# Optimization experiments

Measured on AMD Instinct MI355X. Metric: run time of the kernel, lower is better.

## Reference

```python
import jax, jax.numpy as jnp
import numpy as np

D_MODEL = 1024
N_HEADS = 8
D_KEYS = 128
D_LLM = 4096


def setup_inputs() -> dict:
    key = jax.random.key(0)
    ks = jax.random.split(key, 12)
    B, L, S = 8, 1024, 1000
    dk = D_KEYS * N_HEADS  # 1024
    inp = {
        "target_embedding": jax.random.normal(ks[0], (B, L, D_MODEL), jnp.float32),
        "source_embedding": jax.random.normal(ks[1], (S, D_LLM), jnp.float32),
        "value_embedding": jax.random.normal(ks[2], (S, D_LLM), jnp.float32),
        # nn.Linear weights are [out_features, in_features]
        "Wq": jax.random.normal(ks[3], (dk, D_MODEL), jnp.float32) * 0.02,
        "bq": jnp.zeros((dk,), jnp.float32),
        "Wk": jax.random.normal(ks[4], (dk, D_LLM), jnp.float32) * 0.02,
        "bk": jnp.zeros((dk,), jnp.float32),
        "Wv": jax.random.normal(ks[5], (dk, D_LLM), jnp.float32) * 0.02,
        "bv": jnp.zeros((dk,), jnp.float32),
        "Wo": jax.random.normal(ks[6], (D_LLM, dk), jnp.float32) * 0.02,
        "bo": jnp.zeros((D_LLM,), jnp.float32),
    }
    return inp


def reference(target_embedding, source_embedding, value_embedding,
              Wq, bq, Wk, bk, Wv, bv, Wo, bo):
    B, L, _ = target_embedding.shape
    S, _ = source_embedding.shape
    H, E = N_HEADS, D_KEYS
    # projections (torch Linear: x @ W.T + b)
    q = (target_embedding @ Wq.T + bq).reshape(B, L, H, E)
    k = (source_embedding @ Wk.T + bk).reshape(S, H, E)
    v = (value_embedding @ Wv.T + bv).reshape(S, H, E)
    scale = 1.0 / np.sqrt(E).astype(np.float32)
    # cross-attention of B*L queries over S shared prototypes
    scores = jnp.einsum('blhe,she->bhls', q, k)  # [B,H,L,S]
    A = jax.nn.softmax(scale * scores, axis=-1)  # dropout is identity in eval
    out = jnp.einsum('bhls,she->blhe', A, v).reshape(B, L, H * E)
    return out @ Wo.T + bo  # [B, L, D_LLM]
```

## Files before the change

### kernel.cpp

```cpp
#include <hip/hip_runtime.h>
#include <hip/hip_bf16.h>


typedef __attribute__((ext_vector_type(8))) short short8;
typedef __attribute__((ext_vector_type(4))) short short4v;
typedef __attribute__((ext_vector_type(4))) float f32x4;
typedef __attribute__((ext_vector_type(4))) int int4v;

#define DEVINL static __device__ __forceinline__

DEVINL unsigned short f2bf(float f) {
  union { float f; unsigned u; } v; v.f = f;
  unsigned r = v.u + 0x7FFFu + ((v.u >> 16) & 1u);
  return (unsigned short)(r >> 16);
}

DEVINL f32x4 zero4() { f32x4 z; z[0] = 0.f; z[1] = 0.f; z[2] = 0.f; z[3] = 0.f; return z; }
DEVINL short8 zero8() { short8 z; z[0]=0; z[1]=0; z[2]=0; z[3]=0; z[4]=0; z[5]=0; z[6]=0; z[7]=0; return z; }

DEVINL void load_lds16(const unsigned short* g, unsigned short* l) {
  __builtin_amdgcn_global_load_lds(
      (const __attribute__((address_space(1))) void*)g,
      (__attribute__((address_space(3))) void*)l, 16, 0, 0);
}

__global__ __launch_bounds__(256)
void cvt3_bf16(const float* __restrict__ s0, unsigned short* __restrict__ d0, int n0,
               const float* __restrict__ s1, unsigned short* __restrict__ d1, int n1,
               const float* __restrict__ s2, unsigned short* __restrict__ d2, int n2)
{
  int idx = (blockIdx.x * 256 + threadIdx.x) * 8;
  const float* s; unsigned short* d; int rel = idx;
  if (rel < n0) { s = s0; d = d0; }
  else {
    rel -= n0;
    if (rel < n1) { s = s1; d = d1; }
    else { rel -= n1; if (rel >= n2) return; s = s2; d = d2; }
  }
  f32x4 x0 = *(const f32x4*)(s + rel);
  f32x4 x1 = *(const f32x4*)(s + rel + 4);
  short8 o;
#pragma unroll
  for (int j = 0; j < 4; j++) { o[j] = (short)f2bf(x0[j]); o[4 + j] = (short)f2bf(x1[j]); }
  *(short8*)(d + rel) = o;
}

template<bool C_BF16>
__global__ __launch_bounds__(256)
void gemm_bb(const unsigned short* __restrict__ A,
             const unsigned short* __restrict__ B,
             const float* __restrict__ bias, float cscale, void* __restrict__ C_,
             int M, int N, int K)
{
  __shared__ unsigned short As[4096];
  __shared__ unsigned short Bs[4096];
  const int t = threadIdx.x;
  const int lane = t & 63, w = t >> 6;
  const int wm = w >> 1, wn = w & 1;
  const int l15 = lane & 15, l4 = lane >> 4;
  const int m0 = blockIdx.y * 128, n0 = blockIdx.x * 128;

  const int srow = w * 32 + (lane >> 2);
  const int scol = (lane & 3) * 8;
  const unsigned short* Ap = A + (size_t)(m0 + srow) * K + scol;
  const unsigned short* Bp = B + (size_t)(n0 + srow) * K + scol;
  unsigned short* AsW = &As[w * 1024];
  unsigned short* BsW = &Bs[w * 1024];

  f32x4 acc[4][4];
#pragma unroll
  for (int i = 0; i < 4; i++)
#pragma unroll
    for (int j = 0; j < 4; j++) acc[i][j] = zero4();

  for (int k0 = 0; k0 < K; k0 += 32) {
    if (k0) __syncthreads();
    load_lds16(Ap + k0, AsW);
    load_lds16(Ap + k0 + (size_t)16 * K, AsW + 512);
    load_lds16(Bp + k0, BsW);
    load_lds16(Bp + k0 + (size_t)16 * K, BsW + 512);
    __syncthreads();

    short8 af[4], bf[4];
#pragma unroll
    for (int mt = 0; mt < 4; mt++)
      af[mt] = *(const short8*)&As[(wm * 64 + mt * 16 + l15) * 32 + l4 * 8];
#pragma unroll
    for (int nt = 0; nt < 4; nt++)
      bf[nt] = *(const short8*)&Bs[(wn * 64 + nt * 16 + l15) * 32 + l4 * 8];
#pragma unroll
    for (int mt = 0; mt < 4; mt++)
#pragma unroll
      for (int nt = 0; nt < 4; nt++)
        acc[mt][nt] = __builtin_amdgcn_mfma_f32_16x16x32_bf16(af[mt], bf[nt], acc[mt][nt], 0, 0, 0);
  }

#pragma unroll
  for (int nt = 0; nt < 4; nt++) {
    const int col = n0 + wn * 64 + nt * 16 + l15;
    const float bvv = bias[col];
#pragma unroll
    for (int mt = 0; mt < 4; mt++) {
#pragma unroll
      for (int j = 0; j < 4; j++) {
        const int row = m0 + wm * 64 + mt * 16 + l4 * 4 + j;
        const float val = (acc[mt][nt][j] + bvv) * cscale;
        if constexpr (C_BF16)
          ((unsigned short*)C_)[(size_t)row * N + col] = f2bf(val);
        else
          ((float*)C_)[(size_t)row * N + col] = val;
      }
    }
  }
}

template<bool A_BF16, bool C_BF16, bool C_T>
__global__ __launch_bounds__(256)
void gemm_bt(const void* __restrict__ A_, const float* __restrict__ B,
             const float* __restrict__ bias, float cscale, void* __restrict__ C_,
             int M, int N, int K)
{
  __shared__ unsigned short As[128][40];
  __shared__ unsigned short Bs[128][40];
  const int t = threadIdx.x;
  const int lane = t & 63, w = t >> 6;
  const int wm = w >> 1, wn = w & 1;
  const int l15 = lane & 15, l4 = lane >> 4;
  const int m0 = blockIdx.y * 128, n0 = blockIdx.x * 128;
  const int srow = t >> 1, scol = (t & 1) * 16;

  f32x4 acc[4][4];
#pragma unroll
  for (int i = 0; i < 4; i++)
#pragma unroll
    for (int j = 0; j < 4; j++) acc[i][j] = zero4();

  const int am = m0 + srow;
  const int bn = n0 + srow;

  for (int k0 = 0; k0 < K; k0 += 32) {
    short8 av0, av1, bv0, bv1;
    if constexpr (A_BF16) {
      const unsigned short* A = (const unsigned short*)A_;
      if (am < M) {
        const unsigned short* p = A + (size_t)am * K + k0 + scol;
        av0 = *(const short8*)p;
        av1 = *(const short8*)(p + 8);
      } else { av0 = zero8(); av1 = zero8(); }
    } else {
      const float* A = (const float*)A_;
      if (am < M) {
        const float* p = A + (size_t)am * K + k0 + scol;
        f32x4 x0 = *(const f32x4*)(p);
        f32x4 x1 = *(const f32x4*)(p + 4);
        f32x4 x2 = *(const f32x4*)(p + 8);
        f32x4 x3 = *(const f32x4*)(p + 12);
#pragma unroll
        for (int i = 0; i < 4; i++) {
          av0[i]     = (short)f2bf(x0[i]);
          av0[4 + i] = (short)f2bf(x1[i]);
          av1[i]     = (short)f2bf(x2[i]);
          av1[4 + i] = (short)f2bf(x3[i]);
        }
      } else { av0 = zero8(); av1 = zero8(); }
    }
    {
      const float* p = B + (size_t)bn * K + k0 + scol;
      f32x4 x0 = *(const f32x4*)(p);
      f32x4 x1 = *(const f32x4*)(p + 4);
      f32x4 x2 = *(const f32x4*)(p + 8);
      f32x4 x3 = *(const f32x4*)(p + 12);
#pragma unroll
      for (int i = 0; i < 4; i++) {
        bv0[i]     = (short)f2bf(x0[i]);
        bv0[4 + i] = (short)f2bf(x1[i]);
        bv1[i]     = (short)f2bf(x2[i]);
        bv1[4 + i] = (short)f2bf(x3[i]);
      }
    }
    __syncthreads();
    *(short8*)&As[srow][scol]     = av0;
    *(short8*)&As[srow][scol + 8] = av1;
    *(short8*)&Bs[srow][scol]     = bv0;
    *(short8*)&Bs[srow][scol + 8] = bv1;
    __syncthreads();

    short8 af[4], bf[4];
#pragma unroll
    for (int mt = 0; mt < 4; mt++)
      af[mt] = *(const short8*)&As[wm * 64 + mt * 16 + l15][l4 * 8];
#pragma unroll
    for (int nt = 0; nt < 4; nt++)
      bf[nt] = *(const short8*)&Bs[wn * 64 + nt * 16 + l15][l4 * 8];
#pragma unroll
    for (int mt = 0; mt < 4; mt++)
#pragma unroll
      for (int nt = 0; nt < 4; nt++)
        acc[mt][nt] = __builtin_amdgcn_mfma_f32_16x16x32_bf16(af[mt], bf[nt], acc[mt][nt], 0, 0, 0);
  }

#pragma unroll
  for (int nt = 0; nt < 4; nt++) {
    const int col = n0 + wn * 64 + nt * 16 + l15;
    const float bvv = bias[col];
#pragma unroll
    for (int mt = 0; mt < 4; mt++) {
#pragma unroll
      for (int j = 0; j < 4; j++) {
        const int row = m0 + wm * 64 + mt * 16 + l4 * 4 + j;
        if (row < M) {
          float val = (acc[mt][nt][j] + bvv) * cscale;
          if constexpr (C_T)
            ((unsigned short*)C_)[(size_t)col * 1024 + row] = f2bf(val);
          else if constexpr (C_BF16)
            ((unsigned short*)C_)[(size_t)row * N + col] = f2bf(val);
          else
            ((float*)C_)[(size_t)row * N + col] = val;
        }
      }
    }
  }
}

__global__ __launch_bounds__(256)
void gemm_splitk_kv(const float* __restrict__ Src, const float* __restrict__ Val,
                    const float* __restrict__ Wk, const float* __restrict__ Wv,
                    float* __restrict__ Pt, int M, int N, int Ktot)
{
  __shared__ unsigned short As[128][40];
  __shared__ unsigned short Bs[128][40];
  const int t = threadIdx.x;
  const int lane = t & 63, w = t >> 6;
  const int wm = w >> 1, wn = w & 1;
  const int l15 = lane & 15, l4 = lane >> 4;
  const int m0 = blockIdx.y * 128, n0 = blockIdx.x * 128;
  const int srow = t >> 1, scol = (t & 1) * 16;

  const int split = blockIdx.z & 3;
  const int tensor = blockIdx.z >> 2;
  const float* A = tensor ? Val : Src;
  const float* B = tensor ? Wv : Wk;
  const int kchunk = Ktot >> 2;
  const int k_begin = split * kchunk;
  const int k_end = k_begin + kchunk;

  f32x4 acc[4][4];
#pragma unroll
  for (int i = 0; i < 4; i++)
#pragma unroll
    for (int j = 0; j < 4; j++) acc[i][j] = zero4();

  const int am = m0 + srow;
  const int bn = n0 + srow;

  for (int k0 = k_begin; k0 < k_end; k0 += 32) {
    short8 av0, av1, bv0, bv1;
    if (am < M) {
      const float* p = A + (size_t)am * Ktot + k0 + scol;
      f32x4 x0 = *(const f32x4*)(p);
      f32x4 x1 = *(const f32x4*)(p + 4);
      f32x4 x2 = *(const f32x4*)(p + 8);
      f32x4 x3 = *(const f32x4*)(p + 12);
#pragma unroll
      for (int i = 0; i < 4; i++) {
        av0[i]     = (short)f2bf(x0[i]);
        av0[4 + i] = (short)f2bf(x1[i]);
        av1[i]     = (short)f2bf(x2[i]);
        av1[4 + i] = (short)f2bf(x3[i]);
      }
    } else { av0 = zero8(); av1 = zero8(); }
    {
      const float* p = B + (size_t)bn * Ktot + k0 + scol;
      f32x4 x0 = *(const f32x4*)(p);
      f32x4 x1 = *(const f32x4*)(p + 4);
      f32x4 x2 = *(const f32x4*)(p + 8);
      f32x4 x3 = *(const f32x4*)(p + 12);
#pragma unroll
      for (int i = 0; i < 4; i++) {
        bv0[i]     = (short)f2bf(x0[i]);
        bv0[4 + i] = (short)f2bf(x1[i]);
        bv1[i]     = (short)f2bf(x2[i]);
        bv1[4 + i] = (short)f2bf(x3[i]);
      }
    }
    __syncthreads();
    *(short8*)&As[srow][scol]     = av0;
    *(short8*)&As[srow][scol + 8] = av1;
    *(short8*)&Bs[srow][scol]     = bv0;
    *(short8*)&Bs[srow][scol + 8] = bv1;
    __syncthreads();

    short8 af[4], bf[4];
#pragma unroll
    for (int mt = 0; mt < 4; mt++)
      af[mt] = *(const short8*)&As[wm * 64 + mt * 16 + l15][l4 * 8];
#pragma unroll
    for (int nt = 0; nt < 4; nt++)
      bf[nt] = *(const short8*)&Bs[wn * 64 + nt * 16 + l15][l4 * 8];
#pragma unroll
    for (int mt = 0; mt < 4; mt++)
#pragma unroll
      for (int nt = 0; nt < 4; nt++)
        acc[mt][nt] = __builtin_amdgcn_mfma_f32_16x16x32_bf16(af[mt], bf[nt], acc[mt][nt], 0, 0, 0);
  }

  if (tensor == 0) {
    float* C = Pt + (size_t)split * 1024000;
#pragma unroll
    for (int nt = 0; nt < 4; nt++) {
      const int col = n0 + wn * 64 + nt * 16 + l15;
#pragma unroll
      for (int mt = 0; mt < 4; mt++) {
#pragma unroll
        for (int j = 0; j < 4; j++) {
          const int row = m0 + wm * 64 + mt * 16 + l4 * 4 + j;
          if (row < M)
            C[(size_t)row * N + col] = acc[mt][nt][j];
        }
      }
    }
  } else {
    float* C = Pt + 4096000 + (size_t)split * 1048576;
#pragma unroll
    for (int nt = 0; nt < 4; nt++) {
      const int col = n0 + wn * 64 + nt * 16 + l15;
#pragma unroll
      for (int mt = 0; mt < 4; mt++) {
        const int row0 = m0 + wm * 64 + mt * 16 + l4 * 4;
        *(f32x4*)&C[(size_t)col * 1024 + row0] = acc[mt][nt];
      }
    }
  }
}

__global__ __launch_bounds__(256)
void reduce_kv2(const float* __restrict__ Pt, const float* __restrict__ bk,
                const float* __restrict__ bv, unsigned short* __restrict__ Kb,
                unsigned short* __restrict__ Vt)
{
  const int bid = blockIdx.x;
  const int t = threadIdx.x;
  if (bid < 1000) {
    const int v4 = bid * 256 + t;
    const float* base = Pt + (size_t)v4 * 4;
    f32x4 s = *(const f32x4*)(base);
#pragma unroll
    for (int sp = 1; sp < 4; sp++) {
      f32x4 p = *(const f32x4*)(base + (size_t)sp * 1024000);
      s[0] += p[0]; s[1] += p[1]; s[2] += p[2]; s[3] += p[3];
    }
    const int col0 = (v4 * 4) & 1023;
    f32x4 bb = *(const f32x4*)(bk + col0);
    short4v o;
#pragma unroll
    for (int j = 0; j < 4; j++) o[j] = (short)f2bf(s[j] + bb[j]);
    *(short4v*)(Kb + (size_t)v4 * 4) = o;
  } else {
    const int v4 = (bid - 1000) * 256 + t;
    const float* base = Pt + 4096000 + (size_t)v4 * 4;
    f32x4 s = *(const f32x4*)(base);
#pragma unroll
    for (int sp = 1; sp < 4; sp++) {
      f32x4 p = *(const f32x4*)(base + (size_t)sp * 1048576);
      s[0] += p[0]; s[1] += p[1]; s[2] += p[2]; s[3] += p[3];
    }
    const int n = (v4 * 4) >> 10;
    const float bb = bv[n];
    short4v o;
#pragma unroll
    for (int j = 0; j < 4; j++) o[j] = (short)f2bf(s[j] + bb);
    *(short4v*)(Vt + (size_t)v4 * 4) = o;
  }
}

__global__ __launch_bounds__(256, 2)
void attn_fused4(const unsigned short* __restrict__ Q,
                 const unsigned short* __restrict__ Kb,
                 const unsigned short* __restrict__ Vt,
                 unsigned short* __restrict__ Ob)
{
  __shared__ unsigned short Ks[2][32][136];
  __shared__ unsigned short Vs[2][128][40];

  const int t = threadIdx.x;
  const int lane = t & 63, w = t >> 6;
  const int g = lane >> 4, q = lane & 15;
  const int qt = blockIdx.x & 7, bh = blockIdx.x >> 3;
  const int b = bh >> 3, h = bh & 7;
  const int qrow0 = b * 1024 + qt * 128 + w * 32;

  const unsigned short* Kh = Kb + h * 128;
  const unsigned short* Vh = Vt + (size_t)h * 128 * 1024;

  short8 qf[2][4];
#pragma unroll
  for (int qn = 0; qn < 2; qn++) {
    const unsigned short* qp = Q + (size_t)(qrow0 + qn * 16 + q) * 1024 + h * 128;
#pragma unroll
    for (int kk = 0; kk < 4; kk++)
      qf[qn][kk] = *(const short8*)(qp + kk * 32 + g * 8);
  }

  f32x4 o[2][8];
#pragma unroll
  for (int qn = 0; qn < 2; qn++)
#pragma unroll
    for (int et = 0; et < 8; et++) o[qn][et] = zero4();
  float m_s[2] = {-__builtin_inff(), -__builtin_inff()};
  float l_s[2] = {0.f, 0.f};

  const int krow = t >> 3, kcol = (t & 7) * 16;
  const int vrow = t >> 1, vcol = (t & 1) * 16;

  {
    const unsigned short* kp = Kh + (size_t)min(krow, 999) * 1024 + kcol;
    short8 ka0 = *(const short8*)kp, ka1 = *(const short8*)(kp + 8);
    const unsigned short* vp = Vh + (size_t)vrow * 1024 + vcol;
    short8 va0 = *(const short8*)vp, va1 = *(const short8*)(vp + 8);
    *(short8*)&Ks[0][krow][kcol]     = ka0;
    *(short8*)&Ks[0][krow][kcol + 8] = ka1;
    *(short8*)&Vs[0][vrow][vcol]     = va0;
    *(short8*)&Vs[0][vrow][vcol + 8] = va1;
  }
  __syncthreads();

  int cur = 0;
  for (int tile = 0; tile < 32; ++tile) {
    const int s0 = tile * 32;
    const bool last = (s0 == 992);

    const int s0n = last ? 992 : s0 + 32;
    const unsigned short* kp = Kh + (size_t)min(s0n + krow, 999) * 1024 + kcol;
    short8 ka0 = *(const short8*)kp, ka1 = *(const short8*)(kp + 8);
    const unsigned short* vp = Vh + (size_t)vrow * 1024 + s0n + vcol;
    short8 va0 = *(const short8*)vp, va1 = *(const short8*)(vp + 8);

    short8 kf[2][4];
#pragma unroll
    for (int sc = 0; sc < 2; sc++)
#pragma unroll
      for (int kk = 0; kk < 4; kk++)
        kf[sc][kk] = *(const short8*)&Ks[cur][sc * 16 + q][kk * 32 + g * 8];

    f32x4 st[2][2];
    __builtin_amdgcn_s_setprio(1);
#pragma unroll
    for (int qn = 0; qn < 2; qn++)
#pragma unroll
      for (int sc = 0; sc < 2; sc++) {
        st[qn][sc] = zero4();
#pragma unroll
        for (int kk = 0; kk < 4; kk++)
          st[qn][sc] = __builtin_amdgcn_mfma_f32_16x16x32_bf16(kf[sc][kk], qf[qn][kk], st[qn][sc], 0, 0, 0);
      }
    __builtin_amdgcn_s_setprio(0);

    short8 vf[8];
#pragma unroll
    for (int et = 0; et < 8; et++)
      vf[et] = *(const short8*)&Vs[cur][et * 16 + q][g * 8];

#pragma unroll
    for (int qn = 0; qn < 2; qn++) {
      float a[8];
#pragma unroll
      for (int sc = 0; sc < 2; sc++)
#pragma unroll
        for (int j = 0; j < 4; j++) {
          float v = st[qn][sc][j];
          if (last) {
            const int sl = s0 + sc * 16 + 4 * g + j;
            v = (sl < 1000) ? v : -__builtin_inff();
          }
          a[sc * 4 + j] = v;
        }
      float pmax = fmaxf(fmaxf(fmaxf(a[0], a[1]), fmaxf(a[2], a[3])),
                         fmaxf(fmaxf(a[4], a[5]), fmaxf(a[6], a[7])));
      pmax = fmaxf(pmax, __shfl_xor(pmax, 16));
      pmax = fmaxf(pmax, __shfl_xor(pmax, 32));
      if (!__all(pmax - m_s[qn] <= 8.0f)) {
        const float mn = fmaxf(m_s[qn], pmax);
        const float alpha = __expf(m_s[qn] - mn);
        m_s[qn] = mn;
        l_s[qn] *= alpha;
#pragma unroll
        for (int et = 0; et < 8; et++)
#pragma unroll
          for (int j = 0; j < 4; j++) o[qn][et][j] *= alpha;
      }
      float e8[8];
#pragma unroll
      for (int k = 0; k < 8; k++) e8[k] = __expf(a[k] - m_s[qn]);
      float rs = ((e8[0] + e8[1]) + (e8[2] + e8[3])) + ((e8[4] + e8[5]) + (e8[6] + e8[7]));
      rs += __shfl_xor(rs, 16);
      rs += __shfl_xor(rs, 32);
      l_s[qn] += rs;

      int D0, D1, D2, D3;
      asm("v_cvt_pk_bf16_f32 %0, %1, %2" : "=v"(D0) : "v"(e8[0]), "v"(e8[1]));
      asm("v_cvt_pk_bf16_f32 %0, %1, %2" : "=v"(D1) : "v"(e8[2]), "v"(e8[3]));
      asm("v_cvt_pk_bf16_f32 %0, %1, %2" : "=v"(D2) : "v"(e8[4]), "v"(e8[5]));
      asm("v_cvt_pk_bf16_f32 %0, %1, %2" : "=v"(D3) : "v"(e8[6]), "v"(e8[7]));
      const int sA = q + ((g & 1) << 5);
      const int sB = sA + 16;
      const int a0 = __shfl(D0, sA), a1 = __shfl(D1, sA);
      const int a2 = __shfl(D2, sA), a3 = __shfl(D3, sA);
      const int b0 = __shfl(D0, sB), b1 = __shfl(D1, sB);
      const int b2 = __shfl(D2, sB), b3 = __shfl(D3, sB);
      const bool hi = (g >= 2);
      int4v pi;
      pi[0] = hi ? a2 : a0;
      pi[1] = hi ? a3 : a1;
      pi[2] = hi ? b2 : b0;
      pi[3] = hi ? b3 : b1;
      const short8 pf = __builtin_bit_cast(short8, pi);

      __builtin_amdgcn_s_setprio(1);
#pragma unroll
      for (int et = 0; et < 8; et++)
        o[qn][et] = __builtin_amdgcn_mfma_f32_16x16x32_bf16(vf[et], pf, o[qn][et], 0, 0, 0);
      __builtin_amdgcn_s_setprio(0);
    }

    *(short8*)&Ks[cur ^ 1][krow][kcol]     = ka0;
    *(short8*)&Ks[cur ^ 1][krow][kcol + 8] = ka1;
    *(short8*)&Vs[cur ^ 1][vrow][vcol]     = va0;
    *(short8*)&Vs[cur ^ 1][vrow][vcol + 8] = va1;
    __syncthreads();
    cur ^= 1;
  }

#pragma unroll
  for (int qn = 0; qn < 2; qn++) {
    const float inv = 1.0f / l_s[qn];
    unsigned short* op = Ob + (size_t)(qrow0 + qn * 16 + q) * 1024 + h * 128;
#pragma unroll
    for (int et = 0; et < 8; et++) {
      short4v o4;
#pragma unroll
      for (int j = 0; j < 4; j++) o4[j] = (short)f2bf(o[qn][et][j] * inv);
      *(short4v*)(op + et * 16 + 4 * g) = o4;
    }
  }
}

extern "C" void kernel_launch(void* const* d_in, const int* in_sizes, int n_in,
                              void* d_out, int out_size, void* d_ws, size_t ws_size,
                              hipStream_t stream) {
  const float* target = (const float*)d_in[0];
  const float* source = (const float*)d_in[1];
  const float* value  = (const float*)d_in[2];
  const float* Wq = (const float*)d_in[3];
  const float* bq = (const float*)d_in[4];
  const float* Wk = (const float*)d_in[5];
  const float* bk = (const float*)d_in[6];
  const float* Wv = (const float*)d_in[7];
  const float* bv = (const float*)d_in[8];
  const float* Wo = (const float*)d_in[9];
  const float* bo = (const float*)d_in[10];
  float* out = (float*)d_out;

  const float SCALE = 0.08838834764831843f;

  char* ws = (char*)d_ws;
  unsigned short* Qb  = (unsigned short*)(ws);
  unsigned short* Kb  = (unsigned short*)(ws + 16777216);
  unsigned short* Vt  = (unsigned short*)(ws + 18825216);
  unsigned short* Tb  = (unsigned short*)(ws + 20922368);
  unsigned short* Ab  = (unsigned short*)(ws + 20922368);
  unsigned short* Wqb = (unsigned short*)(ws + 37699584);
  unsigned short* Wob = (unsigned short*)(ws + 39796736);
  float* Pt = (float*)d_out;
  const size_t WS_NEED = 48185344;

  dim3 blk(256);
  if (ws_size >= WS_NEED) {
    cvt3_bf16<<<dim3(6656), blk, 0, stream>>>(
        target, Tb, 8192 * 1024, Wq, Wqb, 1024 * 1024, Wo, Wob, 4096 * 1024);
    gemm_splitk_kv<<<dim3(8, 8, 8), blk, 0, stream>>>(
        source, value, Wk, Wv, Pt, 1000, 1024, 4096);
    reduce_kv2<<<dim3(2024), blk, 0, stream>>>(Pt, bk, bv, Kb, Vt);
    gemm_bb<true><<<dim3(8, 64), blk, 0, stream>>>(
        Tb, Wqb, bq, SCALE, (void*)Qb, 8192, 1024, 1024);
    attn_fused4<<<dim3(512), blk, 0, stream>>>(Qb, Kb, Vt, Ab);
    gemm_bb<false><<<dim3(32, 64), blk, 0, stream>>>(
        Ab, Wob, bo, 1.0f, (void*)out, 8192, 4096, 1024);
  } else {
    gemm_bt<false, true, false><<<dim3(8, 64), blk, 0, stream>>>(
        (const void*)target, Wq, bq, SCALE, (void*)Qb, 8192, 1024, 1024);
    gemm_splitk_kv<<<dim3(8, 8, 8), blk, 0, stream>>>(
        source, value, Wk, Wv, Pt, 1000, 1024, 4096);
    reduce_kv2<<<dim3(2024), blk, 0, stream>>>(Pt, bk, bv, Kb, Vt);
    attn_fused4<<<dim3(512), blk, 0, stream>>>(Qb, Kb, Vt, Ab);
    gemm_bt<true, false, false><<<dim3(32, 64), blk, 0, stream>>>(
        (const void*)Ab, Wo, bo, 1.0f, (void*)out, 8192, 4096, 1024);
  }
}
```

Baseline: 273.5 us.

## Add 256x256-tile triple-buffered bf16 GEMM for output projection

Replaces the 128x128-tile output projection GEMM with a new 512-thread kernel that computes 256x256 tiles. It uses a 3-stage LDS ring fed by direct global-to-LDS loads with a swizzled layout, an XCD-aware block remap, and setprio around the MFMA block. The larger tile halves global traffic per FLOP and the deeper pipeline hides load latency, at the cost of 96KB LDS per block and heavy register use (128 accumulator floats per lane).

```diff
diff --git a/kernel.cpp b/kernel.cpp
--- a/kernel.cpp
+++ b/kernel.cpp
@@ -43,6 +43,117 @@
 #pragma unroll
   for (int j = 0; j < 4; j++) { o[j] = (short)f2bf(x0[j]); o[4 + j] = (short)f2bf(x1[j]); }
   *(short8*)(d + rel) = o;
+}
+
+__global__ __launch_bounds__(512, 2)
+void gemm256(const unsigned short* __restrict__ A,
+             const unsigned short* __restrict__ B,
+             const float* __restrict__ bias, float cscale,
+             float* __restrict__ C, int M, int N, int K)
+{
+  __shared__ unsigned short lds[49152];
+  const int tid = threadIdx.x;
+  const int lane = tid & 63, w = tid >> 6;
+  const int wr = w >> 2, wc = w & 3;
+  const int l15 = lane & 15, l4 = lane >> 4;
+
+  const int nwg = gridDim.x;
+  const int q8 = nwg >> 3;
+  const int swz = (blockIdx.x & 7) * q8 + (blockIdx.x >> 3);
+  const int nbx = N >> 8;
+  const int bx = swz % nbx, by = swz / nbx;
+  const int m0 = by << 8, n0 = bx << 8;
+
+  const unsigned short* gA[2];
+  const unsigned short* gB[2];
+#pragma unroll
+  for (int i = 0; i < 2; i++) {
+    const int c = i * 512 + tid;
+    const int row = 2 * (c >> 3) + ((c >> 2) & 1);
+    const int k4 = (c & 3) ^ ((c >> 3) & 3);
+    gA[i] = A + (size_t)(m0 + row) * K + k4 * 8;
+    gB[i] = B + (size_t)(n0 + row) * K + k4 * 8;
+  }
+
+  const int e = wr * 128 + l15;
+  const int f = wc * 64 + l15;
+  const unsigned cA0 = ((unsigned)(e >> 1) << 7) + ((e & 1) << 6) + ((l4 ^ ((e >> 1) & 3)) << 4);
+  const unsigned cB0 = 16384u + ((unsigned)(f >> 1) << 7) + ((f & 1) << 6) + ((l4 ^ ((f >> 1) & 3)) << 4);
+  const char* ldsc = (const char*)lds;
+
+  f32x4 acc[8][4];
+#pragma unroll
+  for (int i = 0; i < 8; i++)
+#pragma unroll
+    for (int j = 0; j < 4; j++) acc[i][j] = zero4();
+
+  const int NT = K >> 5;
+
+#pragma unroll
+  for (int pt = 0; pt < 2; pt++) {
+    unsigned short* db = lds + pt * 16384;
+#pragma unroll
+    for (int i = 0; i < 2; i++) {
+      load_lds16(gA[i] + pt * 32, db + (i * 512 + w * 64) * 8);
+      load_lds16(gB[i] + pt * 32, db + ((i + 2) * 512 + w * 64) * 8);
+    }
+  }
+  asm volatile("s_waitcnt vmcnt(4)" ::: "memory");
+  __builtin_amdgcn_sched_barrier(0);
+  __builtin_amdgcn_s_barrier();
+  __builtin_amdgcn_sched_barrier(0);
+
+  int bcur = 0, bstg = 2;
+  for (int t = 0; t < NT; ++t) {
+    if (t + 2 < NT) {
+      unsigned short* db = lds + bstg * 16384;
+      const int kt = (t + 2) * 32;
+#pragma unroll
+      for (int i = 0; i < 2; i++) {
+        load_lds16(gA[i] + kt, db + (i * 512 + w * 64) * 8);
+        load_lds16(gB[i] + kt, db + ((i + 2) * 512 + w * 64) * 8);
+      }
+    }
+    const unsigned bufb = (unsigned)bcur * 32768u;
+    const short8* pA = (const short8*)(ldsc + bufb + cA0);
+    const short8* pB = (const short8*)(ldsc + bufb + cB0);
+    short8 af[8], bfr[4];
+#pragma unroll
+    for (int mt = 0; mt < 8; mt++) af[mt] = pA[mt * 64];
+#pragma unroll
+    for (int nt = 0; nt < 4; nt++) bfr[nt] = pB[nt * 64];
+
+    __builtin_amdgcn_s_setprio(1);
+#pragma unroll
+    for (int mt = 0; mt < 8; mt++)
+#pragma unroll
+      for (int nt = 0; nt < 4; nt++)
+        acc[mt][nt] = __builtin_amdgcn_mfma_f32_16x16x32_bf16(af[mt], bfr[nt], acc[mt][nt], 0, 0, 0);
+    __builtin_amdgcn_s_setprio(0);
+
+    if (t + 1 < NT) {
+      if (t + 2 < NT) asm volatile("s_waitcnt vmcnt(4)" ::: "memory");
+      else            asm volatile("s_waitcnt vmcnt(0)" ::: "memory");
+      __builtin_amdgcn_sched_barrier(0);
+      __builtin_amdgcn_s_barrier();
+      __builtin_amdgcn_sched_barrier(0);
+    }
+    bcur = (bcur == 2) ? 0 : bcur + 1;
+    bstg = (bstg == 2) ? 0 : bstg + 1;
+  }
+
+#pragma unroll
+  for (int nt = 0; nt < 4; nt++) {
+    const int col = n0 + wc * 64 + nt * 16 + l15;
+    const float bvv = bias[col];
+#pragma unroll
+    for (int mt = 0; mt < 8; mt++) {
+      const int row = m0 + wr * 128 + mt * 16 + l4 * 4;
+#pragma unroll
+      for (int j = 0; j < 4; j++)
+        C[(size_t)(row + j) * N + col] = (acc[mt][nt][j] + bvv) * cscale;
+    }
+  }
 }
 
 template<bool C_BF16>
@@ -583,8 +694,8 @@
     gemm_bb<true><<<dim3(8, 64), blk, 0, stream>>>(
         Tb, Wqb, bq, SCALE, (void*)Qb, 8192, 1024, 1024);
     attn_fused4<<<dim3(512), blk, 0, stream>>>(Qb, Kb, Vt, Ab);
-    gemm_bb<false><<<dim3(32, 64), blk, 0, stream>>>(
-        Ab, Wob, bo, 1.0f, (void*)out, 8192, 4096, 1024);
+    gemm256<<<dim3(512), dim3(512), 0, stream>>>(
+        Ab, Wob, bo, 1.0f, out, 8192, 4096, 1024);
   } else {
     gemm_bt<false, true, false><<<dim3(8, 64), blk, 0, stream>>>(
         (const void*)target, Wq, bq, SCALE, (void*)Qb, 8192, 1024, 1024);
```

New measurement: 266.2 us. 2.7% less time.
